# Performance work log

Hardware: AMD Instinct MI355X
Metric: run time of the kernel (lower is better)

Reference implementation:

```python
import jax, jax.numpy as jnp
from jax import lax
import numpy as np

B, T, V, U = 64, 2048, 256, 256
BLANK = 0
NEG = jnp.float32(-1e30)


def setup_inputs() -> dict:
    key = jax.random.key(0)
    k1, k2, k3, k4 = jax.random.split(key, 4)
    logits = jax.random.normal(k1, (B, T, V), dtype=jnp.float32)
    targets = jax.random.randint(k2, (B, U), 1, V)               # labels 1..V-1 (0 = blank)
    targets_lengths = jax.random.randint(k3, (B,), U // 2, U + 1)
    logits_lengths = jax.random.randint(k4, (B,), T // 2, T + 1)
    return dict(logits=logits, targets=targets,
                logits_lengths=logits_lengths, targets_lengths=targets_lengths)


def _ctc_forced_alignment(logp, targets, logits_lengths, targets_lengths):
    """Viterbi forced alignment over the CTC extended state graph.
    Returns per-frame best-path labels, shape [B, T] (get_alignment_3d, is_ctc=True)."""
    Bs, Ts, _ = logp.shape
    Us = targets.shape[1]
    S = 2 * Us + 1
    s_idx = jnp.arange(S)
    # extended sequence: blank, t1, blank, t2, ..., blank
    lab_pos = jnp.minimum(s_idx // 2, Us - 1)
    ext = jnp.where((s_idx % 2 == 1)[None, :], jnp.take(targets, lab_pos, axis=1), BLANK)  # [B,S]
    # emission scores em[b,t,s] = logp[b,t,ext[b,s]]
    em = jnp.take_along_axis(logp, jnp.broadcast_to(ext[:, None, :], (Bs, Ts, S)), axis=2)

    valid = s_idx[None, :] < (2 * targets_lengths[:, None] + 1)              # [B,S]
    ext_m2 = jnp.pad(ext[:, :-2], ((0, 0), (2, 0)), constant_values=BLANK)
    skip_ok = (s_idx[None, :] >= 2) & ((s_idx % 2 == 1)[None, :]) & (ext != ext_m2)

    idx_blank = 2 * targets_lengths          # last blank state (S_b - 1)
    idx_label = 2 * targets_lengths - 1      # last label state (S_b - 2)

    alpha0 = jnp.where(valid & (s_idx[None, :] <= 1), em[:, 0, :], NEG)

    def pair_of(alpha):
        vb = jnp.take_along_axis(alpha, idx_blank[:, None], axis=1)
        vl = jnp.take_along_axis(alpha, idx_label[:, None], axis=1)
        return jnp.concatenate([vb, vl], axis=1)  # [B,2]

    def step(alpha, em_t):
        a1 = jnp.pad(alpha[:, :-1], ((0, 0), (1, 0)), constant_values=NEG)
        a2 = jnp.where(skip_ok, jnp.pad(alpha[:, :-2], ((0, 0), (2, 0)), constant_values=NEG), NEG)
        stacked = jnp.stack([alpha, a1, a2])     # [3,B,S]
        bp = jnp.argmax(stacked, axis=0).astype(jnp.int32)
        alpha_new = jnp.where(valid, jnp.max(stacked, axis=0) + em_t, NEG)
        return alpha_new, (bp, pair_of(alpha_new))

    _, (bps, pairs) = lax.scan(step, alpha0, jnp.moveaxis(em, 1, 0)[1:])
    bps = jnp.concatenate([jnp.zeros((1, Bs, S), jnp.int32), bps])            # [T,B,S]
    pairs = jnp.concatenate([pair_of(alpha0)[None], pairs])                   # [T,B,2]

    last_pair = pairs[logits_lengths - 1, jnp.arange(Bs)]                     # value at final valid frame
    end_state = jnp.where(last_pair[:, 0] >= last_pair[:, 1], idx_blank, idx_label).astype(jnp.int32)

    def back(s, inp):
        t, bp_t = inp
        label = jnp.take_along_axis(ext, s[:, None], axis=1)[:, 0]
        step_bp = jnp.take_along_axis(bp_t, s[:, None], axis=1)[:, 0]
        s_prev = jnp.where(t - 1 >= logits_lengths - 1, end_state, s - step_bp)
        return s_prev.astype(jnp.int32), label

    ts = jnp.arange(Ts - 1, -1, -1)
    _, labels_rev = lax.scan(back, end_state, (ts, bps[::-1]))
    return labels_rev[::-1].T  # [B,T] per-frame aligned target labels


def reference(logits, targets, logits_lengths, targets_lengths):
    logp = jax.nn.log_softmax(logits, axis=2)                                 # [B,T,V]
    aligned = lax.stop_gradient(
        _ctc_forced_alignment(logp, targets, logits_lengths, targets_lengths))
    nll = -jnp.take_along_axis(logp, aligned[:, :, None], axis=2)[..., 0]     # [B,T]
    mask = (jnp.arange(logp.shape[1])[None, :] < logits_lengths[:, None]).astype(logp.dtype)
    # reduce=True: mean over valid (unmasked) positions
    return jnp.sum(nll * mask) / jnp.sum(mask)
```

## Files before the change

### kernel.cpp

```cpp
#include <hip/hip_runtime.h>

#define NEGF -1e30f
typedef unsigned int uint32;

static constexpr int Bb = 64, Tt = 2048, Vv = 256, Uu = 256;

__device__ __forceinline__ unsigned short f2bf(float f) {
  uint32 u = __builtin_bit_cast(uint32, f);
  u += 0x7fffu + ((u >> 16) & 1u);
  return (unsigned short)(u >> 16);
}
__device__ __forceinline__ float bf2f_lo(uint32 p) { return __builtin_bit_cast(float, p << 16); }
__device__ __forceinline__ float bf2f_hi(uint32 p) { return __builtin_bit_cast(float, p & 0xffff0000u); }

__device__ __forceinline__ float dpp_shr1(float old, float src) {
  return __builtin_bit_cast(float, __builtin_amdgcn_update_dpp(
      __builtin_bit_cast(int, old), __builtin_bit_cast(int, src), 0x138, 0xF, 0xF, false));
}
__device__ __forceinline__ float dpp_shl1(float old, float src) {
  return __builtin_bit_cast(float, __builtin_amdgcn_update_dpp(
      __builtin_bit_cast(int, old), __builtin_bit_cast(int, src), 0x130, 0xF, 0xF, false));
}

__global__ __launch_bounds__(256) void gather_lse_kernel(
    const float* __restrict__ logits, const int* __restrict__ targets,
    const int* __restrict__ llen, float* __restrict__ gpart,
    float* __restrict__ Ebs, unsigned short* __restrict__ E) {
  __shared__ __align__(16) float buf[4][8][Vv];
  __shared__ float wpart[4];
  const int b = blockIdx.x >> 5;
  const int c = blockIdx.x & 31;
  const int w = threadIdx.x >> 6;
  const int lane = threadIdx.x & 63;
  const int L = llen[b];
  const int4 lb = reinterpret_cast<const int4*>(targets + (b << 8))[lane];
  const float* __restrict__ lgb = logits + (size_t)b * (Tt * Vv);
  float lse_local = 0.f;
#pragma unroll
  for (int k = 0; k < 2; ++k) {
    const int tbase = (c << 6) + (k << 5) + w;
    if (tbase >= L) break;
    float4 v[8];
#pragma unroll
    for (int j = 0; j < 8; ++j)
      v[j] = reinterpret_cast<const float4*>(lgb + (size_t)(tbase + 4 * j) * Vv)[lane];
    float s[8];
#pragma unroll
    for (int j = 0; j < 8; ++j)
      s[j] = __expf(v[j].x) + __expf(v[j].y) + __expf(v[j].z) + __expf(v[j].w);
#pragma unroll
    for (int off = 32; off; off >>= 1) {
#pragma unroll
      for (int j = 0; j < 8; ++j) s[j] += __shfl_down(s[j], off);
    }
#pragma unroll
    for (int j = 0; j < 8; ++j)
      reinterpret_cast<float4*>(&buf[w][j][0])[lane] = v[j];
#pragma unroll
    for (int j = 0; j < 8; ++j) {
      const int t = tbase + 4 * j;
      const bool val = t < L;
      const float bl = buf[w][j][0];
      ushort4 o;
      o.x = f2bf(buf[w][j][lb.x] - bl); o.y = f2bf(buf[w][j][lb.y] - bl);
      o.z = f2bf(buf[w][j][lb.z] - bl); o.w = f2bf(buf[w][j][lb.w] - bl);
      if (val)
        reinterpret_cast<ushort4*>(E + ((size_t)((b << 11) + t)) * Vv)[lane] = o;
      if ((lane == 0) & val) {
        lse_local += __logf(s[j]);
        Ebs[(b << 11) + ((t == 0) ? 2047 : t - 1)] = v[j].x;
      }
    }
  }
  if (lane == 0) wpart[w] = lse_local;
  __syncthreads();
  if (threadIdx.x == 0)
    gpart[blockIdx.x] = wpart[0] + wpart[1] + wpart[2] + wpart[3];
}

#define PG 8
__global__ __launch_bounds__(128) void viterbi_kernel(
    const unsigned short* __restrict__ E, const float* __restrict__ Ebs,
    const int* __restrict__ targets, const int* __restrict__ llen,
    const int* __restrict__ tlen, float* __restrict__ vpart) {
  __shared__ __align__(16) float LB[2048];
  __shared__ float Bt[520];
  const int b = blockIdx.x;
  const int lane = threadIdx.x & 63;
  const int wv = threadIdx.x >> 6;
  const int L = llen[b];
  const int tl = tlen[b];
  const int M = (L - 2) >> 1;
  const int4 lb = reinterpret_cast<const int4*>(targets + (b << 8))[lane];
  const uint2* __restrict__ Erow = reinterpret_cast<const uint2*>(E) + ((size_t)(b << 11) << 6);
  const float* __restrict__ Ebb = Ebs + (b << 11);

  {
    const float4* src = reinterpret_cast<const float4*>(Ebb);
    float4* dst = reinterpret_cast<float4*>(LB);
    for (int i = threadIdx.x; i < 512; i += 128) dst[i] = src[i];
  }
  __syncthreads();

  float a0 = NEGF, a1 = NEGF, a2 = NEGF, a3 = NEGF, a4 = NEGF,
        a5 = NEGF, a6 = NEGF, a7 = NEGF, a8 = NEGF;

  if (wv == 0) {
    const int prevw = __shfl_up(lb.w, 1);
    const bool sk0 = (lane != 0) && (lb.x != prevw);
    const bool sk1 = (lb.y != lb.x);
    const bool sk2 = (lb.z != lb.y);
    const bool sk3 = (lb.w != lb.z);
    if (lane == 0) {
      a0 = 0.f;
      a1 = bf2f_lo((uint32)*reinterpret_cast<const unsigned short*>(E + ((size_t)(b << 11) << 8)));
    }
    uint2 pf[PG][4];
    auto fetchf = [&](int slot, int k) {
      const int kk = (k > 511) ? 511 : k;
#pragma unroll
      for (int j = 0; j < 4; ++j) {
        int r = 1 + 4 * kk + j; r = (r > 2047) ? 2047 : r;
        pf[slot][j] = Erow[(size_t)(r << 6) + lane];
      }
    };
    auto stepf = [&](uint2 em) {
      const float e0 = bf2f_lo(em.x), e1 = bf2f_hi(em.x);
      const float e2 = bf2f_lo(em.y), e3 = bf2f_hi(em.y);
      const float am1 = dpp_shr1(NEGF, a7);
      const float x0 = fmaxf(a0, am1);
      const float x1 = fmaxf(fmaxf(a1, a0), sk0 ? am1 : NEGF) + e0;
      const float x2 = fmaxf(a2, a1);
      const float x3 = fmaxf(fmaxf(a3, a2), sk1 ? a1 : NEGF) + e1;
      const float x4 = fmaxf(a4, a3);
      const float x5 = fmaxf(fmaxf(a5, a4), sk2 ? a3 : NEGF) + e2;
      const float x6 = fmaxf(a6, a5);
      const float x7 = fmaxf(fmaxf(a7, a6), sk3 ? a5 : NEGF) + e3;
      const float x8 = fmaxf(a8, a7);
      a0 = x0; a1 = x1; a2 = x2; a3 = x3; a4 = x4; a5 = x5; a6 = x6; a7 = x7; a8 = x8;
    };
    const int n = M, Gf = n >> 2, remf = n & 3;
#pragma unroll
    for (int s = 0; s < PG; ++s) fetchf(s, s);
    __builtin_amdgcn_sched_barrier(0);
    int g = 0;
    while (g + PG <= Gf) {
#pragma unroll
      for (int s = 0; s < PG; ++s) {
#pragma unroll
        for (int j = 0; j < 4; ++j) stepf(pf[s][j]);
        fetchf(s, g + s + PG);
        __builtin_amdgcn_sched_barrier(0);
      }
      g += PG;
    }
    const int left = Gf - g;
#pragma unroll
    for (int s = 0; s < PG; ++s) {
      if (s < left) {
#pragma unroll
        for (int j = 0; j < 4; ++j) stepf(pf[s][j]);
      }
    }
#pragma unroll
    for (int s = 0; s < PG; ++s) {
      if (s == left) {
#pragma unroll
        for (int j = 0; j < 4; ++j)
          if (j < remf) stepf(pf[s][j]);
      }
    }
  } else {
    const int nlabx = __shfl_down(lb.x, 1);
    const bool kb0 = (lb.y != lb.x);
    const bool kb1 = (lb.z != lb.y);
    const bool kb2 = (lb.w != lb.z);
    const bool kb3 = (lane < 63) && (nlabx != lb.w);
    {
      const uint2 er = Erow[(size_t)((L - 1) << 6) + lane];
      const float e0 = bf2f_lo(er.x), e1 = bf2f_hi(er.x);
      const float e2 = bf2f_lo(er.y), e3 = bf2f_hi(er.y);
      const int s0 = 8 * lane, tb = 2 * tl, tm = 2 * tl - 1;
      a0 = (s0     == tb) ? 0.f : NEGF;
      a1 = (s0 + 1 == tm) ? e0  : NEGF;
      a2 = (s0 + 2 == tb) ? 0.f : NEGF;
      a3 = (s0 + 3 == tm) ? e1  : NEGF;
      a4 = (s0 + 4 == tb) ? 0.f : NEGF;
      a5 = (s0 + 5 == tm) ? e2  : NEGF;
      a6 = (s0 + 6 == tb) ? 0.f : NEGF;
      a7 = (s0 + 7 == tm) ? e3  : NEGF;
      a8 = ((lane == 63) && (tb == 512)) ? 0.f : NEGF;
    }
    uint2 qf[PG][4];
    auto fetchb = [&](int slot, int k) {
#pragma unroll
      for (int j = 0; j < 4; ++j) {
        int r = L - 2 - 4 * k - j; r = (r < 1) ? 1 : r;
        qf[slot][j] = Erow[(size_t)(r << 6) + lane];
      }
    };
    auto stepb = [&](uint2 em) {
      const float e0 = bf2f_lo(em.x), e1 = bf2f_hi(em.x);
      const float e2 = bf2f_lo(em.y), e3 = bf2f_hi(em.y);
      const float bn0 = dpp_shl1(a8, a0);
      const float bn1 = dpp_shl1(NEGF, a1);
      const float y0 = fmaxf(a0, a1);
      const float y1 = fmaxf(fmaxf(a1, a2), kb0 ? a3 : NEGF) + e0;
      const float y2 = fmaxf(a2, a3);
      const float y3 = fmaxf(fmaxf(a3, a4), kb1 ? a5 : NEGF) + e1;
      const float y4 = fmaxf(a4, a5);
      const float y5 = fmaxf(fmaxf(a5, a6), kb2 ? a7 : NEGF) + e2;
      const float y6 = fmaxf(a6, a7);
      const float y7 = fmaxf(fmaxf(a7, bn0), kb3 ? bn1 : NEGF) + e3;
      a0 = y0; a1 = y1; a2 = y2; a3 = y3; a4 = y4; a5 = y5; a6 = y6; a7 = y7;
    };
    const int n = L - 2 - M, Gb = n >> 2, remb = n & 3;
#pragma unroll
    for (int s = 0; s < PG; ++s) fetchb(s, s);
    __builtin_amdgcn_sched_barrier(0);
    int g = 0;
    while (g + PG <= Gb) {
#pragma unroll
      for (int s = 0; s < PG; ++s) {
#pragma unroll
        for (int j = 0; j < 4; ++j) stepb(qf[s][j]);
        fetchb(s, g + s + PG);
        __builtin_amdgcn_sched_barrier(0);
      }
      g += PG;
    }
    const int left = Gb - g;
#pragma unroll
    for (int s = 0; s < PG; ++s) {
      if (s < left) {
#pragma unroll
        for (int j = 0; j < 4; ++j) stepb(qf[s][j]);
      }
    }
#pragma unroll
    for (int s = 0; s < PG; ++s) {
      if (s == left) {
#pragma unroll
        for (int j = 0; j < 4; ++j)
          if (j < remb) stepb(qf[s][j]);
      }
    }
    Bt[8 * lane + 0] = a0; Bt[8 * lane + 1] = a1;
    Bt[8 * lane + 2] = a2; Bt[8 * lane + 3] = a3;
    Bt[8 * lane + 4] = a4; Bt[8 * lane + 5] = a5;
    Bt[8 * lane + 6] = a6; Bt[8 * lane + 7] = a7;
    if (lane == 63) Bt[512] = a8;
    if (lane == 0) { Bt[513] = NEGF; Bt[514] = NEGF; }
  }
  __syncthreads();
  if (wv == 0) {
    const int nlabx = __shfl_down(lb.x, 1);
    const bool kb0 = (lb.y != lb.x);
    const bool kb1 = (lb.z != lb.y);
    const bool kb2 = (lb.w != lb.z);
    const bool kb3 = (lane < 63) && (nlabx != lb.w);
    const int s0 = 8 * lane;
    float best;
    best =             a0 + fmaxf(Bt[s0],     Bt[s0 + 1]);
    best = fmaxf(best, a1 + fmaxf(fmaxf(Bt[s0 + 1], Bt[s0 + 2]), kb0 ? Bt[s0 + 3] : NEGF));
    best = fmaxf(best, a2 + fmaxf(Bt[s0 + 2], Bt[s0 + 3]));
    best = fmaxf(best, a3 + fmaxf(fmaxf(Bt[s0 + 3], Bt[s0 + 4]), kb1 ? Bt[s0 + 5] : NEGF));
    best = fmaxf(best, a4 + fmaxf(Bt[s0 + 4], Bt[s0 + 5]));
    best = fmaxf(best, a5 + fmaxf(fmaxf(Bt[s0 + 5], Bt[s0 + 6]), kb2 ? Bt[s0 + 7] : NEGF));
    best = fmaxf(best, a6 + fmaxf(Bt[s0 + 6], Bt[s0 + 7]));
    best = fmaxf(best, a7 + fmaxf(fmaxf(Bt[s0 + 7], Bt[s0 + 8]), kb3 ? Bt[s0 + 9] : NEGF));
    best = fmaxf(best, a8 + Bt[512]);
    float csum = 0.f;
#pragma unroll
    for (int i = 0; i < 32; ++i) {
      const int idx = lane + (i << 6);
      csum += (idx <= L - 2) ? LB[idx] : 0.f;
    }
#pragma unroll
    for (int off = 32; off; off >>= 1) {
      best = fmaxf(best, __shfl_down(best, off));
      csum += __shfl_down(csum, off);
    }
    if (lane == 0) vpart[b] = best + csum + LB[2047];
  }
}

__global__ __launch_bounds__(256) void finalize_kernel(
    const int* __restrict__ llen, const float* __restrict__ gpart,
    const float* __restrict__ vpart, float* __restrict__ out) {
  __shared__ float sred[4], lred[4];
  const int t = threadIdx.x, lane = t & 63, w = t >> 6;
  float s = 0.f;
#pragma unroll
  for (int i = 0; i < 8; ++i) s += gpart[t + (i << 8)];
  float lf = 0.f;
  if (t < 64) { s -= vpart[t]; lf = (float)llen[t]; }
#pragma unroll
  for (int off = 32; off; off >>= 1) {
    s += __shfl_down(s, off);
    lf += __shfl_down(lf, off);
  }
  if (lane == 0) { sred[w] = s; lred[w] = lf; }
  __syncthreads();
  if (t == 0)
    out[0] = (sred[0] + sred[1] + sred[2] + sred[3]) /
             (lred[0] + lred[1] + lred[2] + lred[3]);
}

extern "C" void kernel_launch(void* const* d_in, const int* in_sizes, int n_in,
                              void* d_out, int out_size, void* d_ws, size_t ws_size,
                              hipStream_t stream) {
  const float* logits  = (const float*)d_in[0];
  const int*   targets = (const int*)d_in[1];
  const int*   llen    = (const int*)d_in[2];
  const int*   tlen    = (const int*)d_in[3];
  float* out = (float*)d_out;

  float*          gpart = (float*)d_ws;
  float*          vpart = (float*)d_ws + 2048;
  float*          Ebs   = (float*)((char*)d_ws + 16384);
  unsigned short* E     = (unsigned short*)((char*)d_ws + (1u << 20));

  gather_lse_kernel<<<Bb * 32, 256, 0, stream>>>(logits, targets, llen, gpart, Ebs, E);
  viterbi_kernel<<<Bb, 128, 0, stream>>>(E, Ebs, targets, llen, tlen, vpart);
  finalize_kernel<<<1, 256, 0, stream>>>(llen, gpart, vpart, out);
}
```

Measured before the change: 260.4 us.

## Interleave emission rows in groups of four and switch to fp16 with mixed-precision adds

Emission scores are now stored in fp16 and in a layout where each lane's four consecutive frames are contiguous, so the Viterbi recurrence loads 16-byte vectors that cover four timesteps instead of separate 8-byte loads per frame. The bf16 unpacking is replaced by v_fma_mix_f32, which adds an fp16 half directly into an fp32 accumulator and saves a conversion instruction per state. The producer kernel now assigns each wave eight consecutive frames so it can write the interleaved layout. The risks are fp16 range and precision on the log-probability differences, and more complex alignment and prologue handling at sequence boundaries.

```diff
diff --git a/kernel.cpp b/kernel.cpp
--- a/kernel.cpp
+++ b/kernel.cpp
@@ -5,13 +5,27 @@
 
 static constexpr int Bb = 64, Tt = 2048, Vv = 256, Uu = 256;
 
-__device__ __forceinline__ unsigned short f2bf(float f) {
-  uint32 u = __builtin_bit_cast(uint32, f);
-  u += 0x7fffu + ((u >> 16) & 1u);
-  return (unsigned short)(u >> 16);
-}
-__device__ __forceinline__ float bf2f_lo(uint32 p) { return __builtin_bit_cast(float, p << 16); }
-__device__ __forceinline__ float bf2f_hi(uint32 p) { return __builtin_bit_cast(float, p & 0xffff0000u); }
+__device__ __forceinline__ unsigned short f2h(float f) {
+  return __builtin_bit_cast(unsigned short, (_Float16)f);
+}
+__device__ __forceinline__ float fp16lo(uint32 w) {
+  return (float)__builtin_bit_cast(_Float16, (unsigned short)(w & 0xffffu));
+}
+__device__ __forceinline__ float fp16hi(uint32 w) {
+  return (float)__builtin_bit_cast(_Float16, (unsigned short)(w >> 16));
+}
+__device__ __forceinline__ float addmix_lo(float acc, uint32 w) {
+  float d;
+  asm("v_fma_mix_f32 %0, %1, 1.0, %2 op_sel:[0,0,0] op_sel_hi:[1,0,0]"
+      : "=v"(d) : "v"(w), "v"(acc));
+  return d;
+}
+__device__ __forceinline__ float addmix_hi(float acc, uint32 w) {
+  float d;
+  asm("v_fma_mix_f32 %0, %1, 1.0, %2 op_sel:[1,0,0] op_sel_hi:[1,0,0]"
+      : "=v"(d) : "v"(w), "v"(acc));
+  return d;
+}
 
 __device__ __forceinline__ float dpp_shr1(float old, float src) {
   return __builtin_bit_cast(float, __builtin_amdgcn_update_dpp(
@@ -35,15 +49,16 @@
   const int L = llen[b];
   const int4 lb = reinterpret_cast<const int4*>(targets + (b << 8))[lane];
   const float* __restrict__ lgb = logits + (size_t)b * (Tt * Vv);
+  unsigned short* __restrict__ Eb2 = E + ((size_t)b << 19);
   float lse_local = 0.f;
 #pragma unroll
   for (int k = 0; k < 2; ++k) {
-    const int tbase = (c << 6) + (k << 5) + w;
+    const int tbase = (c << 6) + (k << 5) + (w << 3);
     if (tbase >= L) break;
     float4 v[8];
 #pragma unroll
     for (int j = 0; j < 8; ++j)
-      v[j] = reinterpret_cast<const float4*>(lgb + (size_t)(tbase + 4 * j) * Vv)[lane];
+      v[j] = reinterpret_cast<const float4*>(lgb + (size_t)(tbase + j) * Vv)[lane];
     float s[8];
 #pragma unroll
     for (int j = 0; j < 8; ++j)
@@ -58,14 +73,14 @@
       reinterpret_cast<float4*>(&buf[w][j][0])[lane] = v[j];
 #pragma unroll
     for (int j = 0; j < 8; ++j) {
-      const int t = tbase + 4 * j;
+      const int t = tbase + j;
       const bool val = t < L;
       const float bl = buf[w][j][0];
       ushort4 o;
-      o.x = f2bf(buf[w][j][lb.x] - bl); o.y = f2bf(buf[w][j][lb.y] - bl);
-      o.z = f2bf(buf[w][j][lb.z] - bl); o.w = f2bf(buf[w][j][lb.w] - bl);
+      o.x = f2h(buf[w][j][lb.x] - bl); o.y = f2h(buf[w][j][lb.y] - bl);
+      o.z = f2h(buf[w][j][lb.z] - bl); o.w = f2h(buf[w][j][lb.w] - bl);
       if (val)
-        reinterpret_cast<ushort4*>(E + ((size_t)((b << 11) + t)) * Vv)[lane] = o;
+        *reinterpret_cast<ushort4*>(Eb2 + (size_t)(t >> 2) * 1024 + (lane << 4) + ((t & 3) << 2)) = o;
       if ((lane == 0) & val) {
         lse_local += __logf(s[j]);
         Ebs[(b << 11) + ((t == 0) ? 2047 : t - 1)] = v[j].x;
@@ -92,8 +107,11 @@
   const int tl = tlen[b];
   const int M = (L - 2) >> 1;
   const int4 lb = reinterpret_cast<const int4*>(targets + (b << 8))[lane];
-  const uint2* __restrict__ Erow = reinterpret_cast<const uint2*>(E) + ((size_t)(b << 11) << 6);
+  const unsigned short* __restrict__ Eb2 = E + ((size_t)b << 19);
   const float* __restrict__ Ebb = Ebs + (b << 11);
+  auto ldrow = [&](int r) {
+    return *reinterpret_cast<const uint2*>(Eb2 + (size_t)(r >> 2) * 1024 + (lane << 4) + ((r & 3) << 2));
+  };
 
   {
     const float4* src = reinterpret_cast<const float4*>(Ebb);
@@ -113,43 +131,41 @@
     const bool sk3 = (lb.w != lb.z);
     if (lane == 0) {
       a0 = 0.f;
-      a1 = bf2f_lo((uint32)*reinterpret_cast<const unsigned short*>(E + ((size_t)(b << 11) << 8)));
-    }
-    uint2 pf[PG][4];
-    auto fetchf = [&](int slot, int k) {
-      const int kk = (k > 511) ? 511 : k;
-#pragma unroll
-      for (int j = 0; j < 4; ++j) {
-        int r = 1 + 4 * kk + j; r = (r > 2047) ? 2047 : r;
-        pf[slot][j] = Erow[(size_t)(r << 6) + lane];
-      }
-    };
-    auto stepf = [&](uint2 em) {
-      const float e0 = bf2f_lo(em.x), e1 = bf2f_hi(em.x);
-      const float e2 = bf2f_lo(em.y), e3 = bf2f_hi(em.y);
+      a1 = fp16lo((uint32)Eb2[0]);
+    }
+    auto stepf = [&](uint32 wx, uint32 wy) {
       const float am1 = dpp_shr1(NEGF, a7);
       const float x0 = fmaxf(a0, am1);
-      const float x1 = fmaxf(fmaxf(a1, a0), sk0 ? am1 : NEGF) + e0;
+      const float x1 = addmix_lo(fmaxf(fmaxf(a1, a0), sk0 ? am1 : NEGF), wx);
       const float x2 = fmaxf(a2, a1);
-      const float x3 = fmaxf(fmaxf(a3, a2), sk1 ? a1 : NEGF) + e1;
+      const float x3 = addmix_hi(fmaxf(fmaxf(a3, a2), sk1 ? a1 : NEGF), wx);
       const float x4 = fmaxf(a4, a3);
-      const float x5 = fmaxf(fmaxf(a5, a4), sk2 ? a3 : NEGF) + e2;
+      const float x5 = addmix_lo(fmaxf(fmaxf(a5, a4), sk2 ? a3 : NEGF), wy);
       const float x6 = fmaxf(a6, a5);
-      const float x7 = fmaxf(fmaxf(a7, a6), sk3 ? a5 : NEGF) + e3;
+      const float x7 = addmix_hi(fmaxf(fmaxf(a7, a6), sk3 ? a5 : NEGF), wy);
       const float x8 = fmaxf(a8, a7);
       a0 = x0; a1 = x1; a2 = x2; a3 = x3; a4 = x4; a5 = x5; a6 = x6; a7 = x7; a8 = x8;
     };
-    const int n = M, Gf = n >> 2, remf = n & 3;
-#pragma unroll
-    for (int s = 0; s < PG; ++s) fetchf(s, s);
+    uint4 pf[PG][2];
+    const uint4* pq = reinterpret_cast<const uint4*>(Eb2 + 1024) + (lane << 1);
+    auto fetchf = [&](int slot) { pf[slot][0] = pq[0]; pf[slot][1] = pq[1]; pq += 128; };
+#pragma unroll
+    for (int s = 0; s < PG; ++s) fetchf(s);
+    {
+      const uint2 w1 = ldrow(1), w2 = ldrow(2), w3 = ldrow(3);
+      stepf(w1.x, w1.y); stepf(w2.x, w2.y); stepf(w3.x, w3.y);
+    }
     __builtin_amdgcn_sched_barrier(0);
+    const int n = M - 3, Gf = n >> 2, remf = n & 3;
     int g = 0;
     while (g + PG <= Gf) {
 #pragma unroll
       for (int s = 0; s < PG; ++s) {
-#pragma unroll
-        for (int j = 0; j < 4; ++j) stepf(pf[s][j]);
-        fetchf(s, g + s + PG);
+        stepf(pf[s][0].x, pf[s][0].y);
+        stepf(pf[s][0].z, pf[s][0].w);
+        stepf(pf[s][1].x, pf[s][1].y);
+        stepf(pf[s][1].z, pf[s][1].w);
+        fetchf(s);
         __builtin_amdgcn_sched_barrier(0);
       }
       g += PG;
@@ -158,16 +174,18 @@
 #pragma unroll
     for (int s = 0; s < PG; ++s) {
       if (s < left) {
-#pragma unroll
-        for (int j = 0; j < 4; ++j) stepf(pf[s][j]);
+        stepf(pf[s][0].x, pf[s][0].y);
+        stepf(pf[s][0].z, pf[s][0].w);
+        stepf(pf[s][1].x, pf[s][1].y);
+        stepf(pf[s][1].z, pf[s][1].w);
       }
     }
 #pragma unroll
     for (int s = 0; s < PG; ++s) {
       if (s == left) {
-#pragma unroll
-        for (int j = 0; j < 4; ++j)
-          if (j < remf) stepf(pf[s][j]);
+        if (remf > 0) stepf(pf[s][0].x, pf[s][0].y);
+        if (remf > 1) stepf(pf[s][0].z, pf[s][0].w);
+        if (remf > 2) stepf(pf[s][1].x, pf[s][1].y);
       }
     }
   } else {
@@ -177,9 +195,9 @@
     const bool kb2 = (lb.w != lb.z);
     const bool kb3 = (lane < 63) && (nlabx != lb.w);
     {
-      const uint2 er = Erow[(size_t)((L - 1) << 6) + lane];
-      const float e0 = bf2f_lo(er.x), e1 = bf2f_hi(er.x);
-      const float e2 = bf2f_lo(er.y), e3 = bf2f_hi(er.y);
+      const uint2 er = ldrow(L - 1);
+      const float e0 = fp16lo(er.x), e1 = fp16hi(er.x);
+      const float e2 = fp16lo(er.y), e3 = fp16hi(er.y);
       const int s0 = 8 * lane, tb = 2 * tl, tm = 2 * tl - 1;
       a0 = (s0     == tb) ? 0.f : NEGF;
       a1 = (s0 + 1 == tm) ? e0  : NEGF;
@@ -191,40 +209,47 @@
       a7 = (s0 + 7 == tm) ? e3  : NEGF;
       a8 = ((lane == 63) && (tb == 512)) ? 0.f : NEGF;
     }
-    uint2 qf[PG][4];
-    auto fetchb = [&](int slot, int k) {
-#pragma unroll
-      for (int j = 0; j < 4; ++j) {
-        int r = L - 2 - 4 * k - j; r = (r < 1) ? 1 : r;
-        qf[slot][j] = Erow[(size_t)(r << 6) + lane];
-      }
-    };
-    auto stepb = [&](uint2 em) {
-      const float e0 = bf2f_lo(em.x), e1 = bf2f_hi(em.x);
-      const float e2 = bf2f_lo(em.y), e3 = bf2f_hi(em.y);
+    auto stepb = [&](uint32 wx, uint32 wy) {
       const float bn0 = dpp_shl1(a8, a0);
       const float bn1 = dpp_shl1(NEGF, a1);
       const float y0 = fmaxf(a0, a1);
-      const float y1 = fmaxf(fmaxf(a1, a2), kb0 ? a3 : NEGF) + e0;
+      const float y1 = addmix_lo(fmaxf(fmaxf(a1, a2), kb0 ? a3 : NEGF), wx);
       const float y2 = fmaxf(a2, a3);
-      const float y3 = fmaxf(fmaxf(a3, a4), kb1 ? a5 : NEGF) + e1;
+      const float y3 = addmix_hi(fmaxf(fmaxf(a3, a4), kb1 ? a5 : NEGF), wx);
       const float y4 = fmaxf(a4, a5);
-      const float y5 = fmaxf(fmaxf(a5, a6), kb2 ? a7 : NEGF) + e2;
+      const float y5 = addmix_lo(fmaxf(fmaxf(a5, a6), kb2 ? a7 : NEGF), wy);
       const float y6 = fmaxf(a6, a7);
-      const float y7 = fmaxf(fmaxf(a7, bn0), kb3 ? bn1 : NEGF) + e3;
+      const float y7 = addmix_hi(fmaxf(fmaxf(a7, bn0), kb3 ? bn1 : NEGF), wy);
       a0 = y0; a1 = y1; a2 = y2; a3 = y3; a4 = y4; a5 = y5; a6 = y6; a7 = y7;
     };
-    const int n = L - 2 - M, Gb = n >> 2, remb = n & 3;
-#pragma unroll
-    for (int s = 0; s < PG; ++s) fetchb(s, s);
+    const int e = L - 2;
+    const int p = (e + 1) & 3;
+    uint4 qf[PG][2];
+    const int q0 = (e - p) >> 2;
+    const uint4* pq = reinterpret_cast<const uint4*>(Eb2) + ((size_t)q0 << 7) + (lane << 1);
+    auto fetchb = [&](int slot) { qf[slot][0] = pq[0]; qf[slot][1] = pq[1]; pq -= 128; };
+#pragma unroll
+    for (int s = 0; s < PG; ++s) fetchb(s);
+    {
+      uint2 pw0, pw1, pw2;
+      if (p > 0) pw0 = ldrow(e);
+      if (p > 1) pw1 = ldrow(e - 1);
+      if (p > 2) pw2 = ldrow(e - 2);
+      if (p > 0) stepb(pw0.x, pw0.y);
+      if (p > 1) stepb(pw1.x, pw1.y);
+      if (p > 2) stepb(pw2.x, pw2.y);
+    }
     __builtin_amdgcn_sched_barrier(0);
+    const int n = (e - M) - p, Gb = n >> 2, remb = n & 3;
     int g = 0;
     while (g + PG <= Gb) {
 #pragma unroll
       for (int s = 0; s < PG; ++s) {
-#pragma unroll
-        for (int j = 0; j < 4; ++j) stepb(qf[s][j]);
-        fetchb(s, g + s + PG);
+        stepb(qf[s][1].z, qf[s][1].w);
+        stepb(qf[s][1].x, qf[s][1].y);
+        stepb(qf[s][0].z, qf[s][0].w);
+        stepb(qf[s][0].x, qf[s][0].y);
+        fetchb(s);
         __builtin_amdgcn_sched_barrier(0);
       }
       g += PG;
@@ -233,16 +258,18 @@
 #pragma unroll
     for (int s = 0; s < PG; ++s) {
       if (s < left) {
-#pragma unroll
-        for (int j = 0; j < 4; ++j) stepb(qf[s][j]);
+        stepb(qf[s][1].z, qf[s][1].w);
+        stepb(qf[s][1].x, qf[s][1].y);
+        stepb(qf[s][0].z, qf[s][0].w);
+        stepb(qf[s][0].x, qf[s][0].y);
       }
     }
 #pragma unroll
     for (int s = 0; s < PG; ++s) {
       if (s == left) {
-#pragma unroll
-        for (int j = 0; j < 4; ++j)
-          if (j < remb) stepb(qf[s][j]);
+        if (remb > 0) stepb(qf[s][1].z, qf[s][1].w);
+        if (remb > 1) stepb(qf[s][1].x, qf[s][1].y);
+        if (remb > 2) stepb(qf[s][0].z, qf[s][0].w);
       }
     }
     Bt[8 * lane + 0] = a0; Bt[8 * lane + 1] = a1;
```

Measured after the change: 251.7 us. 3.4% less time.
